# Performance work log

Measured on AMD Instinct MI355X. Metric: run time of the kernel, lower is better.

The kernel has to match this reference:

```python
import jax, jax.numpy as jnp
import numpy as np

N = 1024          # num_features
H = N // 2        # core dimension (num_params // 2)
NB = 4            # num_blocks
B = 16384         # batch


def _lifted_core(rot_params, diag_params):
    """Build the (N, N) lifted core matrix for one Cayley block."""
    # skew-symmetric matrix from the H rotation params
    S = rot_params[:, None] - rot_params[None, :]            # (H, H)
    I = jnp.eye(H, dtype=rot_params.dtype)
    rotation = jnp.linalg.solve(I - S, I + S)                # Cayley transform
    core = diag_params[:, None] * rotation                   # diag(d) @ rotation
    # rot90(core, k=o) only depends on o mod 4 -> precompute 4 variants
    rots = jnp.stack([core,
                      jnp.rot90(core, 1),
                      jnp.rot90(core, 2),
                      jnp.rot90(core, 3)])                   # (4, H, H)

    def body(lifted, o):
        blk = jax.lax.dynamic_slice(lifted, (o, o), (H, H)) + rots[o % 4]
        return jax.lax.dynamic_update_slice(lifted, blk, (o, o)), None

    lifted, _ = jax.lax.scan(body, jnp.zeros((N, N), dtype=core.dtype),
                             jnp.arange(H + 1))
    return lifted


def setup_inputs() -> dict:
    key = jax.random.key(0)
    ks = jax.random.split(key, 5)
    x = jax.random.normal(ks[0], (B, N), dtype=jnp.float32)
    enc_rot = jax.random.normal(ks[1], (NB, H), dtype=jnp.float32)
    enc_diag = jax.random.normal(ks[2], (NB, H), dtype=jnp.float32)
    dec_rot = jax.random.normal(ks[3], (NB, H), dtype=jnp.float32)
    dec_diag = jax.random.normal(ks[4], (NB, H), dtype=jnp.float32)
    return {"x": x, "enc_rot": enc_rot, "enc_diag": enc_diag,
            "dec_rot": dec_rot, "dec_diag": dec_diag}


def reference(x, enc_rot, enc_diag, dec_rot, dec_diag):
    s = x
    for i in range(NB):                                      # encoder blocks
        s = s @ _lifted_core(enc_rot[i], enc_diag[i]).T
    bottleneck = s
    out = s
    for i in range(NB):                                      # decoder blocks
        out = out @ _lifted_core(dec_rot[i], dec_diag[i]).T
    return bottleneck, out
```

## Files before the change

### kernel.cpp

```cpp
#include <hip/hip_runtime.h>
#include <hip/hip_bf16.h>
#include <cstdint>
#include <cstddef>

#define H 512
#define NFEAT 1024
#define BATCH 16384
#define LM ((size_t)1 << 20)
#define KOP 576

using bf16 = __hip_bfloat16;
using bf16x8 = __attribute__((ext_vector_type(8))) __bf16;
using f32x4 = __attribute__((ext_vector_type(4))) float;
using f32x16 = __attribute__((ext_vector_type(16))) float;

__device__ __forceinline__ void gload16(void* lds, const void* g) {
  __builtin_amdgcn_global_load_lds(
      (__attribute__((address_space(1))) void*)g,
      (__attribute__((address_space(3))) void*)lds,
      16, 0, 0);
}

__global__ __launch_bounds__(256) void prepfused_kernel(
    const float* __restrict__ er, const float* __restrict__ ed,
    const float* __restrict__ dr, const float* __restrict__ dd,
    float* __restrict__ ab, float* __restrict__ Tpref) {
  __shared__ double sred[256], qred[256];
  __shared__ float sa[512];
  __shared__ float buf[4][512];
  __shared__ float tmp[4][512];

  const int mat = blockIdx.x;
  const int t = threadIdx.x;
  const float* u = (mat < 4) ? (er + mat * H) : (dr + (mat - 4) * H);
  const float* d = (mat < 4) ? (ed + mat * H) : (dd + (mat - 4) * H);

  {
    const double v0 = (double)u[t];
    const double v1 = (double)u[t + 256];
    sred[t] = v0 + v1;
    qred[t] = v0 * v0 + v1 * v1;
  }
  __syncthreads();
  for (int off = 128; off; off >>= 1) {
    if (t < off) {
      sred[t] += sred[t + off];
      qred[t] += qred[t + off];
    }
    __syncthreads();
  }
  const double s = sred[0];
  const double q = qred[0];
  const double det = 1.0 - s * s + (double)H * q;
  const double cuv = 2.0 * (1.0 + s) / det;
  const double cuu = -2.0 * (double)H / det;
  const double cvv = -2.0 * q / det;
  const double cvu = -2.0 * (1.0 - s) / det;

  float* a = ab + mat * 1024;
  float* b = a + H;
#pragma unroll
  for (int h = 0; h < 2; ++h) {
    const int idx = t + 256 * h;
    const double ui = (double)u[idx], di = (double)d[idx];
    const float av = (float)(di * (cuv * ui + cvv));
    const float bv = (float)(di * (cuu * ui + cvu));
    a[idx] = av;
    b[idx] = bv;
    sa[idx] = av;
  }
  __syncthreads();

  for (int m = t; m < 512; m += 256) {
    buf[0][m] = sa[m];
    buf[1][m] = sa[511 - m];
    buf[2][m] = d[m];
    buf[3][m] = d[511 - m];
  }
  __syncthreads();
  for (int st = 4; st <= 256; st <<= 1) {
    for (int m = t; m < 512; m += 256)
#pragma unroll
      for (int qq = 0; qq < 4; ++qq) tmp[qq][m] = (m >= st) ? buf[qq][m - st] : 0.f;
    __syncthreads();
    for (int m = t; m < 512; m += 256)
#pragma unroll
      for (int qq = 0; qq < 4; ++qq) buf[qq][m] += tmp[qq][m];
    __syncthreads();
  }
  float* tp = Tpref + mat * 2048;
  for (int m = t; m < 512; m += 256) {
    tp[m] = buf[0][m];
    tp[512 + m] = buf[1][m];
    tp[1024 + m] = buf[2][m];
    tp[1536 + m] = buf[3][m];
  }
}

__global__ __launch_bounds__(256) void genops_kernel(
    const float* __restrict__ er, const float* __restrict__ dr,
    const float* __restrict__ ab,
    bf16* __restrict__ Ah, bf16* __restrict__ Bh, bf16* __restrict__ Bl,
    const float* __restrict__ x, bf16* __restrict__ Qh) {
  const int xr = blockIdx.x;
  const int mat = blockIdx.y;
  const float* u = (mat < 4) ? (er + mat * H) : (dr + (mat - 4) * H);
  const float* b = ab + mat * 1024 + H;
  const int t = threadIdx.x;
  const size_t base = ((size_t)mat * 1024 + xr) * KOP;
  for (int k = t; k < KOP; k += 256) {
    float av = 0.f, bv = 0.f;
    if (k <= 128) {
      const int o = 4 * k;
      const int ia = xr - o;
      av = (ia >= 0 && ia < 512) ? b[ia] : 0.f;
      bv = (ia >= 0 && ia < 512) ? u[ia] : 0.f;
    } else if (k <= 256) {
      const int o = 4 * (k - 129) + 1;
      const int ia = 511 - xr + o;
      const int ib = xr - o;
      av = (ia >= 0 && ia < 512) ? u[ia] : 0.f;
      bv = (ib >= 0 && ib < 512) ? b[ib] : 0.f;
    } else if (k <= 384) {
      const int o = 4 * (k - 257) + 2;
      const int ia = 511 - xr + o;
      av = (ia >= 0 && ia < 512) ? b[ia] : 0.f;
      bv = (ia >= 0 && ia < 512) ? u[ia] : 0.f;
    } else if (k <= 512) {
      const int o = 4 * (k - 385) + 3;
      const int ia = xr - o;
      const int ib = 511 - xr + o;
      av = (ia >= 0 && ia < 512) ? u[ia] : 0.f;
      bv = (ib >= 0 && ib < 512) ? b[ib] : 0.f;
    }
    Ah[base + k] = __float2bfloat16(av);
    const bf16 bh = __float2bfloat16(bv);
    Bh[base + k] = bh;
    Bl[base + k] = __float2bfloat16(bv - __bfloat162float(bh));
  }

  const int n4 = BATCH * NFEAT / 4;
  const int gidx = (mat * 1024 + xr) * 256 + t;
  for (int i = gidx; i < n4; i += 8192 * 256) {
    float4 v = ((const float4*)x)[i];
    union { bf16 bb[4]; short4 sv; } Hu;
    Hu.bb[0] = __float2bfloat16(v.x);
    Hu.bb[1] = __float2bfloat16(v.y);
    Hu.bb[2] = __float2bfloat16(v.z);
    Hu.bb[3] = __float2bfloat16(v.w);
    ((short4*)Qh)[i] = Hu.sv;
  }
}

__global__ __launch_bounds__(256) void buildgemm_kernel(
    const bf16* __restrict__ Ah, const bf16* __restrict__ Bh,
    const bf16* __restrict__ Bl,
    const float* __restrict__ ed, const float* __restrict__ dd,
    const float* __restrict__ Tpref, bf16* __restrict__ Lbase) {
  __shared__ __align__(16) bf16 smem[3 * 8192];
  __shared__ float pa[512], parev[512], pd[512], pdrev[512], sdl[512];
  bf16* sAh = smem;
  bf16* sBh = smem + 8192;
  bf16* sBl = smem + 16384;

  const int tid = threadIdx.x;
  const int lane = tid & 63;
  const int wave = tid >> 6;
  const int wr = wave >> 1;
  const int wc = wave & 1;
  const int mat = blockIdx.z;
  const int row0 = blockIdx.x * 128;
  const int col0 = blockIdx.y * 128;

  {
    const float* tp = Tpref + mat * 2048;
    const float* d = (mat < 4) ? (ed + mat * H) : (dd + (mat - 4) * H);
    for (int m = tid; m < 512; m += 256) {
      pa[m] = tp[m];
      parev[m] = tp[512 + m];
      pd[m] = tp[1024 + m];
      pdrev[m] = tp[1536 + m];
      sdl[m] = d[m];
    }
  }

  const size_t OPS = (size_t)mat * 1024 * KOP;
  const int srow = tid >> 3;
  const int sce = (((tid * 16) ^ (((tid >> 3) & 7) << 4)) & 127) >> 1;
  const size_t abase = OPS + (size_t)(row0 + srow) * KOP + sce;
  const size_t bbase = OPS + (size_t)(col0 + srow) * KOP + sce;
  const int dst0 = tid * 8;

  f32x16 acc[2][2] = {};

  for (int kt = 0; kt < 9; ++kt) {
    const int k0 = kt * 64;
#pragma unroll
    for (int q = 0; q < 4; ++q) {
      const size_t ga = abase + (size_t)(32 * q) * KOP + k0;
      const size_t gb = bbase + (size_t)(32 * q) * KOP + k0;
      const int dq = q * 2048 + dst0;
      gload16(sAh + dq, Ah + ga);
      gload16(sBh + dq, Bh + gb);
      gload16(sBl + dq, Bl + gb);
    }
    __syncthreads();

    const int l31 = lane & 31;
    const int kh16 = (lane >> 5) * 16;
#pragma unroll
    for (int ks = 0; ks < 4; ++ks) {
      bf16x8 fah[2], fbh[2], fbl[2];
#pragma unroll
      for (int m = 0; m < 2; ++m) {
        const int arow = wr * 64 + m * 32 + l31;
        const int abk = (arow * 128 + ks * 32 + kh16) ^ ((arow & 7) << 4);
        fah[m] = *(const bf16x8*)((const char*)sAh + abk);
        const int brow = wc * 64 + m * 32 + l31;
        const int bbk = (brow * 128 + ks * 32 + kh16) ^ ((brow & 7) << 4);
        fbh[m] = *(const bf16x8*)((const char*)sBh + bbk);
        fbl[m] = *(const bf16x8*)((const char*)sBl + bbk);
      }
#pragma unroll
      for (int m = 0; m < 2; ++m)
#pragma unroll
        for (int n = 0; n < 2; ++n) {
          acc[m][n] = __builtin_amdgcn_mfma_f32_32x32x16_bf16(fah[m], fbh[n], acc[m][n], 0, 0, 0);
          acc[m][n] = __builtin_amdgcn_mfma_f32_32x32x16_bf16(fah[m], fbl[n], acc[m][n], 0, 0, 0);
        }
    }
    __syncthreads();
  }

  auto apart = [&](int i, int j) -> float {
    const int lo = max(0, max(i, j) - 511);
    const int hi = min(512, min(i, j));
    if (lo > hi) return 0.f;
    float v = 0.f;
    {
      int o1 = lo + ((0 - lo) & 3), o2 = hi - (hi & 3);
      if (o1 <= o2) { int mx = i - o1, mn = i - o2; v += pa[mx] - (mn >= 4 ? pa[mn - 4] : 0.f); }
    }
    {
      int o1 = lo + ((1 - lo) & 3), o2 = hi - ((hi - 1) & 3);
      if (o1 <= o2) { int mx = j - o1, mn = j - o2; v += pa[mx] - (mn >= 4 ? pa[mn - 4] : 0.f); }
    }
    {
      int o1 = lo + ((2 - lo) & 3), o2 = hi - ((hi - 2) & 3);
      if (o1 <= o2) { int mx = i - o1, mn = i - o2; v += parev[mx] - (mn >= 4 ? parev[mn - 4] : 0.f); }
    }
    {
      int o1 = lo + ((3 - lo) & 3), o2 = hi - ((hi - 3) & 3);
      if (o1 <= o2) { int mx = j - o1, mn = j - o2; v += parev[mx] - (mn >= 4 ? parev[mn - 4] : 0.f); }
    }
    if (i == j) {
      {
        int o1 = lo + ((0 - lo) & 3), o2 = hi - (hi & 3);
        if (o1 <= o2) { int mx = i - o1, mn = i - o2; v += pd[mx] - (mn >= 4 ? pd[mn - 4] : 0.f); }
      }
      {
        int o1 = lo + ((2 - lo) & 3), o2 = hi - ((hi - 2) & 3);
        if (o1 <= o2) { int mx = i - o1, mn = i - o2; v += pdrev[mx] - (mn >= 4 ? pdrev[mn - 4] : 0.f); }
      }
    }
    const int m2 = i + j - 511;
    if (m2 >= 0 && !(m2 & 1)) {
      const int os = m2 >> 1;
      if (os >= lo && os <= hi) {
        const int r = os & 3;
        if (r == 1) v += sdl[j - os];
        else if (r == 3) v += sdl[511 - (j - os)];
      }
    }
    return v;
  };

  const int ocol0 = col0 + wc * 64 + (lane & 31);
  const int rb = (lane >> 5) << 2;
#pragma unroll
  for (int m = 0; m < 2; ++m)
#pragma unroll
    for (int n = 0; n < 2; ++n)
#pragma unroll
      for (int r = 0; r < 16; ++r) {
        const int grow = row0 + wr * 64 + m * 32 + (r & 3) + ((r >> 2) << 3) + rb;
        const int gcol = ocol0 + n * 32;
        const float v = acc[m][n][r] + apart(grow, gcol);
        const size_t off = ((size_t)mat << 21) + ((size_t)grow << 10) + (size_t)gcol;
        const bf16 hb = __float2bfloat16(v);
        Lbase[off] = hb;
        Lbase[off + LM] = __float2bfloat16(v - __bfloat162float(hb));
      }
}

struct TPtrs { const bf16* s; bf16* d; };
struct T6 { TPtrs t[6]; };

__global__ __launch_bounds__(256) void transposeB_kernel(T6 p) {
  const bf16* S = p.t[blockIdx.z].s;
  bf16* D = p.t[blockIdx.z].d;
  __shared__ ushort tile[64][68];
  const int i0 = blockIdx.x * 64, j0 = blockIdx.y * 64;
  const int tid = threadIdx.x;
  const int rr = tid >> 4;
  const int cc = (tid & 15) * 4;
#pragma unroll
  for (int it = 0; it < 4; ++it) {
    const int row = it * 16 + rr;
    const size_t so = (size_t)(i0 + row) * 1024 + j0 + cc;
    ushort4 v = *(const ushort4*)((const ushort*)S + so);
    tile[row][cc] = v.x; tile[row][cc + 1] = v.y;
    tile[row][cc + 2] = v.z; tile[row][cc + 3] = v.w;
  }
  __syncthreads();
#pragma unroll
  for (int it = 0; it < 4; ++it) {
    const int row = it * 16 + rr;
    ushort4 o;
    o.x = tile[cc][row];     o.y = tile[cc + 1][row];
    o.z = tile[cc + 2][row]; o.w = tile[cc + 3][row];
    const size_t dofs = (size_t)(j0 + row) * 1024 + i0 + cc;
    *(ushort4*)((ushort*)D + dofs) = o;
  }
}

struct GPtrs { const bf16* a; const bf16* b; bf16* yh; bf16* yl; };
struct G4 { GPtrs g[4]; };

__global__ __launch_bounds__(256) void chaingemm4_kernel(G4 p) {
  GPtrs q = p.g[blockIdx.z];
  const bf16* A = q.a;
  const bf16* Bh = q.b;
  const bf16* Bl = q.b + LM;

  __shared__ __align__(16) bf16 smem[3 * 12288];

  const int tid = threadIdx.x;
  const int lane = tid & 63;
  const int wave = tid >> 6;
  const int wr = wave >> 1, wc = wave & 1;
  const int r0 = blockIdx.x * 64, c0 = blockIdx.y * 64;

  const int srow = tid >> 3;
  const int scol = (((tid & 7) ^ (srow & 7))) * 8;
  const int dst = tid * 8;
  const size_t ga0 = (size_t)(r0 + srow) * 1024 + scol;
  const size_t gb0 = (size_t)(c0 + srow) * 1024 + scol;

  auto STAGE = [&](int buf, int k0) {
    bf16* base = smem + buf * 12288;
    gload16(base + dst,        A + ga0 + k0);
    gload16(base + 2048 + dst, A + ga0 + 32 * 1024 + k0);
    gload16(base + 4096 + dst,        Bh + gb0 + k0);
    gload16(base + 4096 + 2048 + dst, Bh + gb0 + 32 * 1024 + k0);
    gload16(base + 8192 + dst,        Bl + gb0 + k0);
    gload16(base + 8192 + 2048 + dst, Bl + gb0 + 32 * 1024 + k0);
  };

  const int l31 = lane & 31;
  const int klg = lane >> 5;
  const int ar = wr * 32 + l31;
  const int br = wc * 32 + l31;
  int aoff[4], boff[4];
#pragma unroll
  for (int ks = 0; ks < 4; ++ks) {
    const int lgA = (ks << 1) | klg;
    aoff[ks] = ar * 64 + ((lgA ^ (ar & 7)) << 3);
    boff[ks] = br * 64 + ((lgA ^ (br & 7)) << 3);
  }

  f32x16 acc = {};

  STAGE(0, 0);
  STAGE(1, 64);
  asm volatile("s_waitcnt vmcnt(6)" ::: "memory");
  __builtin_amdgcn_s_barrier();

  for (int t = 0; t < 16; ++t) {
    const int buf = t % 3;
    if (t < 14) STAGE((t + 2) % 3, (t + 2) * 64);

    const bf16* pA = smem + buf * 12288;
    const bf16* pBh = pA + 4096;
    const bf16* pBl = pA + 8192;
#pragma unroll
    for (int ks = 0; ks < 4; ++ks) {
      bf16x8 ah = *(const bf16x8*)(pA + aoff[ks]);
      bf16x8 bh = *(const bf16x8*)(pBh + boff[ks]);
      bf16x8 bl = *(const bf16x8*)(pBl + boff[ks]);
      acc = __builtin_amdgcn_mfma_f32_32x32x16_bf16(ah, bh, acc, 0, 0, 0);
      acc = __builtin_amdgcn_mfma_f32_32x32x16_bf16(ah, bl, acc, 0, 0, 0);
    }
    if (t <= 13) {
      asm volatile("s_waitcnt vmcnt(6)" ::: "memory");
    } else if (t == 14) {
      asm volatile("s_waitcnt vmcnt(0)" ::: "memory");
    }
    __builtin_amdgcn_s_barrier();
  }

  const int oc = c0 + wc * 32 + l31;
  const int rb = (lane >> 5) << 2;
#pragma unroll
  for (int r = 0; r < 16; ++r) {
    const int gr = r0 + wr * 32 + (r & 3) + ((r >> 2) << 3) + rb;
    const size_t off = (size_t)gr * 1024 + oc;
    const float v = acc[r];
    const bf16 hb = __float2bfloat16(v);
    q.yh[off] = hb;
    q.yl[off] = __float2bfloat16(v - __bfloat162float(hb));
  }
}

__global__ __launch_bounds__(256, 2) void gemmbig_kernel(
    const bf16* __restrict__ A, const bf16* __restrict__ Bh_,
    float* __restrict__ Y0, float* __restrict__ Y1) {
  __shared__ __align__(16) bf16 smem[3 * 12288];

  const int tid = threadIdx.x;
  const int lane = tid & 63;
  const int wave = tid >> 6;
  const int wr = wave >> 1;
  const int wc = wave & 1;

  const int pdisp = blockIdx.x;
  const int xcd = pdisp & 7;
  const int chk = pdisp >> 3;
  const int row0 = (xcd * 16 + (chk >> 3)) * 128;
  const int col0 = (chk & 7) * 256;

  const int sr = tid >> 2;
  const int sc = ((tid & 3) ^ ((tid >> 3) & 3)) * 8;
  const size_t abase0 = (size_t)(row0 + sr) * NFEAT + sc;
  const size_t abase1 = abase0 + (size_t)64 * NFEAT;
  const size_t bbase = (size_t)(col0 + sr) * NFEAT + sc;
  const int dst = tid * 8;

  auto STAGE_A = [&](int buf, int k0) {
    bf16* base = smem + buf * 12288;
    gload16(base + dst, A + abase0 + k0);
    gload16(base + 2048 + dst, A + abase1 + k0);
  };
  auto STAGE_B = [&](int buf, int k0) {
    bf16* base = smem + buf * 12288 + 4096;
#pragma unroll
    for (int q = 0; q < 4; ++q)
      gload16(base + q * 2048 + dst, Bh_ + bbase + (size_t)(64 * q) * NFEAT + k0);
  };

  const int l15 = lane & 15;
  const int kcol = ((lane >> 4) * 16) ^ (((l15 >> 1) & 3) << 4);
  int aoff[4], boff[8];
#pragma unroll
  for (int fr = 0; fr < 4; ++fr)
    aoff[fr] = (wr * 64 + fr * 16 + l15) * 64 + kcol;
#pragma unroll
  for (int fc = 0; fc < 8; ++fc)
    boff[fc] = 8192 + (wc * 128 + fc * 16 + l15) * 64 + kcol;

  auto LD = [&](int buf, int off) {
    return *(const bf16x8*)((const char*)(smem + buf * 12288) + off);
  };

  f32x4 acc[4][8] = {};

  STAGE_A(0, 0); STAGE_B(0, 0);
  STAGE_A(1, 32); STAGE_B(1, 32);
  asm volatile("s_waitcnt vmcnt(6)" ::: "memory");
  __builtin_amdgcn_s_barrier();

  for (int T = 0; T < 32; ++T) {
    const int buf = T % 3;
    if (T < 30) {
      const int nb = (T + 2) % 3;
      STAGE_A(nb, (T + 2) * 32);
      STAGE_B(nb, (T + 2) * 32);
    }

    bf16x8 fa[4], fb[4];
#pragma unroll
    for (int fr = 0; fr < 4; ++fr) fa[fr] = LD(buf, aoff[fr]);
#pragma unroll
    for (int fc = 0; fc < 4; ++fc) fb[fc] = LD(buf, boff[fc]);
    __builtin_amdgcn_s_setprio(1);
#pragma unroll
    for (int fr = 0; fr < 4; ++fr)
#pragma unroll
      for (int fc = 0; fc < 4; ++fc)
        acc[fr][fc] = __builtin_amdgcn_mfma_f32_16x16x32_bf16(fa[fr], fb[fc], acc[fr][fc], 0, 0, 0);
    __builtin_amdgcn_s_setprio(0);
#pragma unroll
    for (int fc = 0; fc < 4; ++fc) fb[fc] = LD(buf, boff[4 + fc]);
    __builtin_amdgcn_s_setprio(1);
#pragma unroll
    for (int fr = 0; fr < 4; ++fr)
#pragma unroll
      for (int fc = 0; fc < 4; ++fc)
        acc[fr][4 + fc] = __builtin_amdgcn_mfma_f32_16x16x32_bf16(fa[fr], fb[fc], acc[fr][4 + fc], 0, 0, 0);
    __builtin_amdgcn_s_setprio(0);

    if (T <= 29) {
      asm volatile("s_waitcnt vmcnt(6)" ::: "memory");
    } else if (T == 30) {
      asm volatile("s_waitcnt vmcnt(0)" ::: "memory");
    }
    __builtin_amdgcn_s_barrier();
  }

  float* Yb = (col0 < 1024) ? Y0 : (Y1 - 1024);
  const int orow = row0 + wr * 64 + (lane >> 4) * 4;
  const int ocol = col0 + wc * 128 + l15;
#pragma unroll
  for (int fr = 0; fr < 4; ++fr)
#pragma unroll
    for (int fc = 0; fc < 8; ++fc)
#pragma unroll
      for (int r = 0; r < 4; ++r) {
        const int grow = orow + fr * 16 + r;
        const int gcol = ocol + fc * 16;
        Yb[(size_t)grow * NFEAT + (size_t)gcol] = acc[fr][fc][r];
      }
}

extern "C" void kernel_launch(void* const* d_in, const int* in_sizes, int n_in,
                              void* d_out, int out_size, void* d_ws, size_t ws_size,
                              hipStream_t stream) {
  (void)in_sizes; (void)n_in; (void)out_size; (void)ws_size;
  const float* x  = (const float*)d_in[0];
  const float* er = (const float*)d_in[1];
  const float* ed = (const float*)d_in[2];
  const float* dr = (const float*)d_in[3];
  const float* dd = (const float*)d_in[4];

  float* O0 = (float*)d_out;
  float* O1 = O0 + (size_t)BATCH * NFEAT;

  bf16* Lb = (bf16*)d_ws;
  float* ab = (float*)(Lb + 16 * LM);
  bf16* Qh = (bf16*)(ab + 8 * 1024);

  float* Tpref = O0;
  bf16* SB = (bf16*)((char*)O0 + (1 << 20));
  auto slot = [&](int s) { return SB + (size_t)s * LM; };

  const size_t OPN = (size_t)8 * 1024 * KOP;
  bf16* Aoph = (bf16*)O1;
  bf16* Boph = Aoph + OPN;
  bf16* Bopl = Boph + OPN;

  prepfused_kernel<<<8, 256, 0, stream>>>(er, ed, dr, dd, ab, Tpref);
  genops_kernel<<<dim3(1024, 8), 256, 0, stream>>>(er, dr, ab, Aoph, Boph, Bopl, x, Qh);
  buildgemm_kernel<<<dim3(8, 8, 8), 256, 0, stream>>>(Aoph, Boph, Bopl,
                                                      ed, dd, Tpref, Lb);

  {
    T6 p;
    p.t[0] = {Lb + 0 * LM,  slot(0)};
    p.t[1] = {Lb + 4 * LM,  slot(2)};
    p.t[2] = {Lb + 5 * LM,  slot(3)};
    p.t[3] = {Lb + 8 * LM,  slot(4)};
    p.t[4] = {Lb + 12 * LM, slot(6)};
    p.t[5] = {Lb + 13 * LM, slot(7)};
    transposeB_kernel<<<dim3(16, 16, 6), 256, 0, stream>>>(p);
  }
  {
    G4 p;
    p.g[0] = {slot(0),      Lb + 2 * LM,  slot(8),  slot(9)};
    p.g[1] = {Lb + 6 * LM,  slot(2),      slot(10), slot(11)};
    p.g[2] = {slot(4),      Lb + 10 * LM, slot(12), slot(13)};
    p.g[3] = {Lb + 14 * LM, slot(6),      slot(14), slot(15)};
    chaingemm4_kernel<<<dim3(16, 16, 4), 256, 0, stream>>>(p);
  }
  {
    G4 p;
    p.g[0] = {slot(8),  slot(10), slot(0), slot(1)};
    p.g[1] = {slot(12), slot(14), slot(2), slot(3)};
    p.g[2] = p.g[0];
    p.g[3] = p.g[1];
    chaingemm4_kernel<<<dim3(16, 16, 2), 256, 0, stream>>>(p);
  }
  {
    T6 p;
    p.t[0] = {slot(0), Lb + 0 * LM};
    p.t[1] = {slot(2), Lb + 2 * LM};
    p.t[2] = p.t[0]; p.t[3] = p.t[0]; p.t[4] = p.t[0]; p.t[5] = p.t[0];
    transposeB_kernel<<<dim3(16, 16, 2), 256, 0, stream>>>(p);
  }
  {
    G4 p;
    p.g[0] = {Lb + 2 * LM, slot(0), Lb + 1 * LM, slot(4)};
    p.g[1] = p.g[0]; p.g[2] = p.g[0]; p.g[3] = p.g[0];
    chaingemm4_kernel<<<dim3(16, 16, 1), 256, 0, stream>>>(p);
  }

  gemmbig_kernel<<<1024, 256, 0, stream>>>(Qh, Lb, O0, O1);
}
```

Before: 238.3 us.

## Enlarge chain GEMM tiles to 128x128 with 16x16x32 MFMA fragments

The chain GEMM kernel that multiplies the 1024x1024 lifted-core matrices now gives each block a 128x128 output tile instead of 64x64. It uses a 32-wide K step with a 4x4 grid of 16x16x32 MFMA accumulators per wave and raises wave priority around the MFMA section. The aim is more reuse per LDS load and fewer global loads per FLOP. The trade-off is that the grid shrinks from 256 to 64 blocks per matrix, which lowers parallelism on a GPU with many CUs, and the accumulators use more registers.

```diff
diff --git a/kernel.cpp b/kernel.cpp
--- a/kernel.cpp
+++ b/kernel.cpp
@@ -327,7 +327,7 @@
 struct GPtrs { const bf16* a; const bf16* b; bf16* yh; bf16* yl; };
 struct G4 { GPtrs g[4]; };
 
-__global__ __launch_bounds__(256) void chaingemm4_kernel(G4 p) {
+__global__ __launch_bounds__(256, 2) void chaingemm5_kernel(G4 p) {
   GPtrs q = p.g[blockIdx.z];
   const bf16* A = q.a;
   const bf16* Bh = q.b;
@@ -338,78 +338,97 @@
   const int tid = threadIdx.x;
   const int lane = tid & 63;
   const int wave = tid >> 6;
-  const int wr = wave >> 1, wc = wave & 1;
-  const int r0 = blockIdx.x * 64, c0 = blockIdx.y * 64;
-
-  const int srow = tid >> 3;
-  const int scol = (((tid & 7) ^ (srow & 7))) * 8;
+  const int wr = wave >> 1;
+  const int wc = wave & 1;
+  const int r0 = blockIdx.x * 128, c0 = blockIdx.y * 128;
+
+  const int sr = tid >> 2;
+  const int sc = ((tid & 3) ^ ((tid >> 3) & 3)) * 8;
+  const size_t abase0 = (size_t)(r0 + sr) * 1024 + sc;
+  const size_t abase1 = abase0 + (size_t)64 * 1024;
+  const size_t bbase0 = (size_t)(c0 + sr) * 1024 + sc;
+  const size_t bbase1 = bbase0 + (size_t)64 * 1024;
   const int dst = tid * 8;
-  const size_t ga0 = (size_t)(r0 + srow) * 1024 + scol;
-  const size_t gb0 = (size_t)(c0 + srow) * 1024 + scol;
 
   auto STAGE = [&](int buf, int k0) {
     bf16* base = smem + buf * 12288;
-    gload16(base + dst,        A + ga0 + k0);
-    gload16(base + 2048 + dst, A + ga0 + 32 * 1024 + k0);
-    gload16(base + 4096 + dst,        Bh + gb0 + k0);
-    gload16(base + 4096 + 2048 + dst, Bh + gb0 + 32 * 1024 + k0);
-    gload16(base + 8192 + dst,        Bl + gb0 + k0);
-    gload16(base + 8192 + 2048 + dst, Bl + gb0 + 32 * 1024 + k0);
+    gload16(base + dst, A + abase0 + k0);
+    gload16(base + 2048 + dst, A + abase1 + k0);
+    gload16(base + 4096 + dst, Bh + bbase0 + k0);
+    gload16(base + 4096 + 2048 + dst, Bh + bbase1 + k0);
+    gload16(base + 8192 + dst, Bl + bbase0 + k0);
+    gload16(base + 8192 + 2048 + dst, Bl + bbase1 + k0);
   };
 
-  const int l31 = lane & 31;
-  const int klg = lane >> 5;
-  const int ar = wr * 32 + l31;
-  const int br = wc * 32 + l31;
-  int aoff[4], boff[4];
-#pragma unroll
-  for (int ks = 0; ks < 4; ++ks) {
-    const int lgA = (ks << 1) | klg;
-    aoff[ks] = ar * 64 + ((lgA ^ (ar & 7)) << 3);
-    boff[ks] = br * 64 + ((lgA ^ (br & 7)) << 3);
-  }
-
-  f32x16 acc = {};
+  const int l15 = lane & 15;
+  const int kcol = ((lane >> 4) * 16) ^ (((l15 >> 1) & 3) << 4);
+  int aoff[4], bhoff[4], bloff[4];
+#pragma unroll
+  for (int fr = 0; fr < 4; ++fr) {
+    const int arow = wr * 64 + fr * 16 + l15;
+    aoff[fr] = arow * 64 + kcol;
+    const int brow = wc * 64 + fr * 16 + l15;
+    bhoff[fr] = 8192 + brow * 64 + kcol;
+    bloff[fr] = 16384 + brow * 64 + kcol;
+  }
+
+  auto LD = [&](int buf, int off) {
+    return *(const bf16x8*)((const char*)(smem + buf * 12288) + off);
+  };
+
+  f32x4 acc[4][4] = {};
 
   STAGE(0, 0);
-  STAGE(1, 64);
+  STAGE(1, 32);
   asm volatile("s_waitcnt vmcnt(6)" ::: "memory");
   __builtin_amdgcn_s_barrier();
 
-  for (int t = 0; t < 16; ++t) {
-    const int buf = t % 3;
-    if (t < 14) STAGE((t + 2) % 3, (t + 2) * 64);
-
-    const bf16* pA = smem + buf * 12288;
-    const bf16* pBh = pA + 4096;
-    const bf16* pBl = pA + 8192;
-#pragma unroll
-    for (int ks = 0; ks < 4; ++ks) {
-      bf16x8 ah = *(const bf16x8*)(pA + aoff[ks]);
-      bf16x8 bh = *(const bf16x8*)(pBh + boff[ks]);
-      bf16x8 bl = *(const bf16x8*)(pBl + boff[ks]);
-      acc = __builtin_amdgcn_mfma_f32_32x32x16_bf16(ah, bh, acc, 0, 0, 0);
-      acc = __builtin_amdgcn_mfma_f32_32x32x16_bf16(ah, bl, acc, 0, 0, 0);
-    }
-    if (t <= 13) {
+  for (int T = 0; T < 32; ++T) {
+    const int buf = T % 3;
+    if (T < 30) STAGE((T + 2) % 3, (T + 2) * 32);
+
+    bf16x8 fa[4], fbh[4], fbl[4];
+#pragma unroll
+    for (int fr = 0; fr < 4; ++fr) fa[fr] = LD(buf, aoff[fr]);
+#pragma unroll
+    for (int fc = 0; fc < 4; ++fc) {
+      fbh[fc] = LD(buf, bhoff[fc]);
+      fbl[fc] = LD(buf, bloff[fc]);
+    }
+    __builtin_amdgcn_s_setprio(1);
+#pragma unroll
+    for (int fr = 0; fr < 4; ++fr)
+#pragma unroll
+      for (int fc = 0; fc < 4; ++fc) {
+        acc[fr][fc] = __builtin_amdgcn_mfma_f32_16x16x32_bf16(fa[fr], fbh[fc], acc[fr][fc], 0, 0, 0);
+        acc[fr][fc] = __builtin_amdgcn_mfma_f32_16x16x32_bf16(fa[fr], fbl[fc], acc[fr][fc], 0, 0, 0);
+      }
+    __builtin_amdgcn_s_setprio(0);
+
+    if (T <= 29) {
       asm volatile("s_waitcnt vmcnt(6)" ::: "memory");
-    } else if (t == 14) {
+    } else if (T == 30) {
       asm volatile("s_waitcnt vmcnt(0)" ::: "memory");
     }
     __builtin_amdgcn_s_barrier();
   }
 
-  const int oc = c0 + wc * 32 + l31;
-  const int rb = (lane >> 5) << 2;
-#pragma unroll
-  for (int r = 0; r < 16; ++r) {
-    const int gr = r0 + wr * 32 + (r & 3) + ((r >> 2) << 3) + rb;
-    const size_t off = (size_t)gr * 1024 + oc;
-    const float v = acc[r];
-    const bf16 hb = __float2bfloat16(v);
-    q.yh[off] = hb;
-    q.yl[off] = __float2bfloat16(v - __bfloat162float(hb));
-  }
+  const int orow = r0 + wr * 64 + (lane >> 4) * 4;
+  const int ocol = c0 + wc * 64 + l15;
+#pragma unroll
+  for (int fr = 0; fr < 4; ++fr)
+#pragma unroll
+    for (int fc = 0; fc < 4; ++fc)
+#pragma unroll
+      for (int r = 0; r < 4; ++r) {
+        const int gr = orow + fr * 16 + r;
+        const int gc = ocol + fc * 16;
+        const size_t off = (size_t)gr * 1024 + gc;
+        const float v = acc[fr][fc][r];
+        const bf16 hb = __float2bfloat16(v);
+        q.yh[off] = hb;
+        q.yl[off] = __float2bfloat16(v - __bfloat162float(hb));
+      }
 }
 
 __global__ __launch_bounds__(256, 2) void gemmbig_kernel(
@@ -569,7 +588,7 @@
     p.g[1] = {Lb + 6 * LM,  slot(2),      slot(10), slot(11)};
     p.g[2] = {slot(4),      Lb + 10 * LM, slot(12), slot(13)};
     p.g[3] = {Lb + 14 * LM, slot(6),      slot(14), slot(15)};
-    chaingemm4_kernel<<<dim3(16, 16, 4), 256, 0, stream>>>(p);
+    chaingemm5_kernel<<<dim3(8, 8, 4), 256, 0, stream>>>(p);
   }
   {
     G4 p;
@@ -577,7 +596,7 @@
     p.g[1] = {slot(12), slot(14), slot(2), slot(3)};
     p.g[2] = p.g[0];
     p.g[3] = p.g[1];
-    chaingemm4_kernel<<<dim3(16, 16, 2), 256, 0, stream>>>(p);
+    chaingemm5_kernel<<<dim3(8, 8, 2), 256, 0, stream>>>(p);
   }
   {
     T6 p;
@@ -590,7 +609,7 @@
     G4 p;
     p.g[0] = {Lb + 2 * LM, slot(0), Lb + 1 * LM, slot(4)};
     p.g[1] = p.g[0]; p.g[2] = p.g[0]; p.g[3] = p.g[0];
-    chaingemm4_kernel<<<dim3(16, 16, 1), 256, 0, stream>>>(p);
+    chaingemm5_kernel<<<dim3(8, 8, 1), 256, 0, stream>>>(p);
   }
 
   gemmbig_kernel<<<1024, 256, 0, stream>>>(Qh, Lb, O0, O1);
```

After: 251.8 us. 5.6% more time.
